# Kernel optimization log

Hardware: AMD Instinct MI355X
Metric: run time of the kernel (lower is better)

Reference implementation:

```python
import jax, jax.numpy as jnp
import numpy as np

N = 100000      # nodes
E = 1600000     # edges (avg degree 16)
F_IN = 64       # graph_input_dim
HID = 64        # gcn_out_dims (constant)
NG = 128        # number of graphs in batch
GF = 32         # global_input_dim
L1, L2, OUT = 256, 128, 1


def _glorot(k, fan_in, fan_out):
    s = 1.0 / np.sqrt(fan_in)
    return jax.random.uniform(k, (fan_in, fan_out), jnp.float32, -s, s)


def setup_inputs() -> dict:
    key = jax.random.key(0)
    ks = jax.random.split(key, 20)
    x = jax.random.normal(ks[0], (N, F_IN), jnp.float32)
    edge_index = jax.random.randint(ks[1], (2, E), 0, N, jnp.int64)
    # every graph gets a contiguous, non-empty slice of nodes (sorted batch ids)
    batch = (jnp.arange(N, dtype=jnp.int64) * NG) // N
    global_features = jax.random.normal(ks[2], (NG, GF), jnp.float32)
    dims = [F_IN, HID, HID, HID]
    inp = {"x": x, "global_features": global_features}
    for i in range(3):
        inp[f"conv_w{i+1}"] = _glorot(ks[3 + i], dims[i], dims[i + 1])
        inp[f"conv_b{i+1}"] = jnp.zeros((dims[i + 1],), jnp.float32)
    inp["fc_w1"] = _glorot(ks[8], HID * 2 + GF, L1)
    inp["fc_b1"] = jnp.zeros((L1,), jnp.float32)
    inp["fc_w2"] = _glorot(ks[9], L1, L2)
    inp["fc_b2"] = jnp.zeros((L2,), jnp.float32)
    inp["out_w"] = _glorot(ks[10], L2, OUT)
    inp["out_b"] = jnp.zeros((OUT,), jnp.float32)
    inp["edge_index"] = edge_index
    inp["batch"] = batch
    return inp


def _gcn_conv(x, src, dst, w, b, n):
    """PyG GCNConv: x' = D^-1/2 (A + I) D^-1/2 (x W) + b."""
    h = x @ w  # [n, out]
    loop = jnp.arange(n, dtype=src.dtype)
    s = jnp.concatenate([src, loop])
    d = jnp.concatenate([dst, loop])
    deg = jax.ops.segment_sum(jnp.ones(s.shape, h.dtype), d, num_segments=n)
    dinv = jnp.where(deg > 0, jax.lax.rsqrt(deg), 0.0)
    norm = dinv[s] * dinv[d]  # [E+n]
    out = jax.ops.segment_sum(h[s] * norm[:, None], d, num_segments=n)
    return out + b


def _forward(x, global_features, conv_w1, conv_b1, conv_w2, conv_b2,
             conv_w3, conv_b3, fc_w1, fc_b1, fc_w2, fc_b2, out_w, out_b,
             edge_index, batch):
    src, dst = edge_index[0], edge_index[1]
    n = x.shape[0]
    ng = global_features.shape[0]
    for w, b in ((conv_w1, conv_b1), (conv_w2, conv_b2), (conv_w3, conv_b3)):
        x = jax.nn.leaky_relu(_gcn_conv(x, src, dst, w, b, n))
    counts = jax.ops.segment_sum(jnp.ones((n,), x.dtype), batch, num_segments=ng)
    mean_pool = jax.ops.segment_sum(x, batch, num_segments=ng) / counts[:, None]
    max_pool = jax.ops.segment_max(x, batch, num_segments=ng)
    h = jnp.concatenate([mean_pool, max_pool, global_features], axis=1)
    h = jax.nn.leaky_relu(h @ fc_w1 + fc_b1)
    h = jax.nn.leaky_relu(h @ fc_w2 + fc_b2)
    return h @ out_w + out_b


def reference(x, global_features, conv_w1, conv_b1, conv_w2, conv_b2,
              conv_w3, conv_b3, fc_w1, fc_b1, fc_w2, fc_b2, out_w, out_b,
              edge_index, batch):
    return _forward(x, global_features, conv_w1, conv_b1, conv_w2, conv_b2,
                    conv_w3, conv_b3, fc_w1, fc_b1, fc_w2, fc_b2, out_w, out_b,
                    edge_index, batch)
```

## Files before the change

### kernel.cpp

```cpp
#include <hip/hip_runtime.h>
#include <hip/hip_fp16.h>
#include <stdint.h>

#define LRELU(x) ((x) > 0.0f ? (x) : 0.01f * (x))

struct h4 { __half2 a, b; };
struct h8 { __half2 a, b, c, d; };

typedef _Float16 f16x8 __attribute__((ext_vector_type(8)));
typedef float    f32x4 __attribute__((ext_vector_type(4)));

#define EPB 8192
#define PARTS 16


__global__ __launch_bounds__(256) void hist1_kernel(const int* __restrict__ dst,
                                                    int* __restrict__ bhist,
                                                    int nblk, int E, int nbk) {
    __shared__ int h[512];
    int blk = blockIdx.x, t = threadIdx.x;
    for (int i = t; i < nbk; i += 256) h[i] = 0;
    __syncthreads();
    #pragma unroll
    for (int k = 0; k < EPB / 1024; ++k) {
        int i4 = blk * (EPB / 4) + k * 256 + t;
        int e = i4 * 4;
        if (e + 3 < E) {
            int4 d = ((const int4*)dst)[i4];
            atomicAdd(&h[d.x >> 8], 1);
            atomicAdd(&h[d.y >> 8], 1);
            atomicAdd(&h[d.z >> 8], 1);
            atomicAdd(&h[d.w >> 8], 1);
        } else {
            for (int j = e; j < E; ++j) atomicAdd(&h[dst[j] >> 8], 1);
        }
    }
    __syncthreads();
    for (int i = t; i < nbk; i += 256) bhist[i * nblk + blk] = h[i];
}

__global__ __launch_bounds__(256) void scanb_kernel(int* __restrict__ bhist,
                                                    int* __restrict__ btot, int nblk) {
    __shared__ int s[256];
    __shared__ int carry;
    int b = blockIdx.x, t = threadIdx.x;
    if (t == 0) carry = 0;
    __syncthreads();
    for (int c0 = 0; c0 < nblk; c0 += 256) {
        int idx = c0 + t;
        int v = (idx < nblk) ? bhist[b * nblk + idx] : 0;
        s[t] = v;
        __syncthreads();
        for (int off = 1; off < 256; off <<= 1) {
            int a = (t >= off) ? s[t - off] : 0;
            __syncthreads();
            s[t] += a;
            __syncthreads();
        }
        if (idx < nblk) bhist[b * nblk + idx] = s[t] - v + carry;
        __syncthreads();
        if (t == 255) carry += s[255];
        __syncthreads();
    }
    if (t == 0) btot[b] = carry;
}

__global__ __launch_bounds__(512) void bbase_wprep_kernel(const int* __restrict__ btot,
                                                          int* __restrict__ bbase,
                                                          int nbk, int E,
                                                          const float* __restrict__ w1,
                                                          const float* __restrict__ w2,
                                                          const float* __restrict__ w3,
                                                          _Float16* __restrict__ Bf) {
    if (blockIdx.x == 0) {
        __shared__ int s[512];
        int t = threadIdx.x;
        int v = (t < nbk) ? btot[t] : 0;
        s[t] = v;
        __syncthreads();
        for (int off = 1; off < 512; off <<= 1) {
            int a = (t >= off) ? s[t - off] : 0;
            __syncthreads();
            s[t] += a;
            __syncthreads();
        }
        if (t < nbk) bbase[t] = s[t] - v;
        if (t == 0) bbase[nbk] = E;
    } else {
        int bc = blockIdx.x - 1;
        int tid = threadIdx.x;
        if (tid < 256) {
            int layer = bc >> 1, c = bc & 1;
            const float* W = (layer == 0) ? w1 : ((layer == 1) ? w2 : w3);
            int t = tid >> 6, l = tid & 63;
            _Float16* dstp = Bf + ((size_t)(layer * 8 + c * 4 + t) * 64 + l) * 8;
            int n  = t * 16 + (l & 15);
            int kb = c * 32 + (l >> 4) * 8;
            #pragma unroll
            for (int i = 0; i < 8; ++i) dstp[i] = (_Float16)W[(kb + i) * 64 + n];
        }
    }
}

__global__ __launch_bounds__(256) void place_kernel(const int* __restrict__ src,
                                                    const int* __restrict__ dst,
                                                    const int* __restrict__ bbase,
                                                    const int* __restrict__ bhist,
                                                    unsigned* __restrict__ bedge,
                                                    int nblk, int E, int nbk) {
    __shared__ int cur[512];
    int blk = blockIdx.x, t = threadIdx.x;
    for (int i = t; i < nbk; i += 256) cur[i] = bbase[i] + bhist[i * nblk + blk];
    __syncthreads();
    #pragma unroll
    for (int k = 0; k < EPB / 1024; ++k) {
        int i4 = blk * (EPB / 4) + k * 256 + t;
        int e = i4 * 4;
        if (e + 3 < E) {
            int4 s4 = ((const int4*)src)[i4];
            int4 d4 = ((const int4*)dst)[i4];
            int p0 = atomicAdd(&cur[d4.x >> 8], 1);
            int p1 = atomicAdd(&cur[d4.y >> 8], 1);
            int p2 = atomicAdd(&cur[d4.z >> 8], 1);
            int p3 = atomicAdd(&cur[d4.w >> 8], 1);
            bedge[p0] = ((unsigned)s4.x << 8) | (unsigned)(d4.x & 255);
            bedge[p1] = ((unsigned)s4.y << 8) | (unsigned)(d4.y & 255);
            bedge[p2] = ((unsigned)s4.z << 8) | (unsigned)(d4.z & 255);
            bedge[p3] = ((unsigned)s4.w << 8) | (unsigned)(d4.w & 255);
        } else {
            for (int j = e; j < E; ++j) {
                int d = dst[j];
                int pos = atomicAdd(&cur[d >> 8], 1);
                bedge[pos] = ((unsigned)src[j] << 8) | (unsigned)(d & 255);
            }
        }
    }
}

__global__ __launch_bounds__(256) void csr_kernel(const unsigned* __restrict__ bedge,
                                                  const int* __restrict__ bbase,
                                                  int* __restrict__ row_ptr,
                                                  float* __restrict__ dinv,
                                                  int* __restrict__ csr_src,
                                                  const int* __restrict__ batch,
                                                  int* __restrict__ gstart,
                                                  int N, int E, int nbk, int NG) {
    __shared__ int cnt[256];
    __shared__ int s[256];
    __shared__ int cur[256];
    int b = blockIdx.x, t = threadIdx.x;
    int node0 = b << 8;
    int beg = bbase[b], end = bbase[b + 1];
    cnt[t] = 0;
    __syncthreads();
    for (int i = beg + t; i < end; i += 256) atomicAdd(&cnt[bedge[i] & 255u], 1);
    __syncthreads();
    int c = cnt[t];
    s[t] = c;
    __syncthreads();
    for (int off = 1; off < 256; off <<= 1) {
        int a = (t >= off) ? s[t - off] : 0;
        __syncthreads();
        s[t] += a;
        __syncthreads();
    }
    int rp = beg + s[t] - c;
    int node = node0 + t;
    if (node < N) {
        row_ptr[node] = rp;
        dinv[node] = rsqrtf((float)c + 1.0f);
        int bb = batch[node];
        if (node == 0) {
            gstart[bb] = 0;
            gstart[NG] = N;
        } else if (batch[node - 1] != bb) {
            gstart[bb] = node;
        }
    }
    cur[t] = rp;
    if (b == nbk - 1 && t == 0) row_ptr[N] = E;
    __syncthreads();
    for (int i = beg + t; i < end; i += 256) {
        unsigned u = bedge[i];
        int pos = atomicAdd(&cur[u & 255u], 1);
        csr_src[pos] = (int)(u >> 8);
    }
}


template <bool XF32>
__global__ __launch_bounds__(256) void gemm_mfma_kernel(const void* __restrict__ Xv,
                                                        const _Float16* __restrict__ Bf,
                                                        const float* __restrict__ dinv,
                                                        __half* __restrict__ H, int N) {
    int w = threadIdx.x >> 6;
    int l = threadIdx.x & 63;
    int col = l & 15;
    int kg  = l >> 4;
    int base = blockIdx.x * 64 + w * 16;
    int nodeA = base + col;
    bool okA = nodeA < N;

    f32x4 acc[4] = {};
    #pragma unroll
    for (int c = 0; c < 2; ++c) {
        int k0 = c * 32 + kg * 8;
        f16x8 a = {};
        if (okA) {
            if constexpr (XF32) {
                const float* xp = (const float*)Xv + (size_t)nodeA * 64 + k0;
                float4 u = *(const float4*)xp;
                float4 v = *(const float4*)(xp + 4);
                a[0] = (_Float16)u.x; a[1] = (_Float16)u.y;
                a[2] = (_Float16)u.z; a[3] = (_Float16)u.w;
                a[4] = (_Float16)v.x; a[5] = (_Float16)v.y;
                a[6] = (_Float16)v.z; a[7] = (_Float16)v.w;
            } else {
                a = *(const f16x8*)((const __half*)Xv + (size_t)nodeA * 64 + k0);
            }
        }
        #pragma unroll
        for (int t = 0; t < 4; ++t) {
            f16x8 b = *(const f16x8*)(Bf + ((size_t)(c * 4 + t) * 64 + l) * 8);
            acc[t] = __builtin_amdgcn_mfma_f32_16x16x32_f16(a, b, acc[t], 0, 0, 0);
        }
    }
    float dvr[4];
    int rowN[4];
    #pragma unroll
    for (int r = 0; r < 4; ++r) {
        rowN[r] = base + kg * 4 + r;
        dvr[r] = (rowN[r] < N) ? dinv[rowN[r]] : 0.0f;
    }
    #pragma unroll
    for (int t = 0; t < 4; ++t) {
        #pragma unroll
        for (int r = 0; r < 4; ++r) {
            if (rowN[r] < N)
                H[(size_t)rowN[r] * 64 + t * 16 + col] = __float2half(acc[t][r] * dvr[r]);
        }
    }
}

#define ACC8(vv, c0, c1, c2, c3, c4, c5, c6, c7)                                \
    { float2 p;                                                                 \
      p = __half22float2((vv).a); c0 += p.x; c1 += p.y;                         \
      p = __half22float2((vv).b); c2 += p.x; c3 += p.y;                         \
      p = __half22float2((vv).c); c4 += p.x; c5 += p.y;                         \
      p = __half22float2((vv).d); c6 += p.x; c7 += p.y; }

__global__ __launch_bounds__(256) void agg_kernel(const __half* __restrict__ H,
                                                  const int* __restrict__ rp,
                                                  const int* __restrict__ csrc,
                                                  const float* __restrict__ dinv,
                                                  const float* __restrict__ bias,
                                                  __half* __restrict__ Y, int N) {
    int w = (blockIdx.x * blockDim.x + threadIdx.x) >> 6;
    int nA = w << 1;
    if (nA >= N) return;
    int nB = nA + 1;
    bool hasB = nB < N;
    int l = threadIdx.x & 63;
    int slot = l >> 3;
    int fo = (l & 7) << 3;
    int endA = rp[nA + 1];
    int eA = rp[nA] + slot;
    int endB = hasB ? rp[nB + 1] : 0;
    int eB = hasB ? (rp[nB] + slot) : 0;
    float a0=0,a1=0,a2=0,a3=0,a4=0,a5=0,a6=0,a7=0;
    float b0=0,b1=0,b2=0,b3=0,b4=0,b5=0,b6=0,b7=0;
    while (eA + 8 < endA && eB + 8 < endB) {
        int sA0 = csrc[eA], sA1 = csrc[eA + 8];
        int sB0 = csrc[eB], sB1 = csrc[eB + 8];
        h8 vA0 = *(const h8*)&H[(size_t)sA0 * 64 + fo];
        h8 vA1 = *(const h8*)&H[(size_t)sA1 * 64 + fo];
        h8 vB0 = *(const h8*)&H[(size_t)sB0 * 64 + fo];
        h8 vB1 = *(const h8*)&H[(size_t)sB1 * 64 + fo];
        ACC8(vA0, a0,a1,a2,a3,a4,a5,a6,a7);
        ACC8(vA1, a0,a1,a2,a3,a4,a5,a6,a7);
        ACC8(vB0, b0,b1,b2,b3,b4,b5,b6,b7);
        ACC8(vB1, b0,b1,b2,b3,b4,b5,b6,b7);
        eA += 16; eB += 16;
    }
    while (eA + 8 < endA) {
        int s0 = csrc[eA], s1 = csrc[eA + 8];
        h8 v0 = *(const h8*)&H[(size_t)s0 * 64 + fo];
        h8 v1 = *(const h8*)&H[(size_t)s1 * 64 + fo];
        ACC8(v0, a0,a1,a2,a3,a4,a5,a6,a7);
        ACC8(v1, a0,a1,a2,a3,a4,a5,a6,a7);
        eA += 16;
    }
    while (eB + 8 < endB) {
        int s0 = csrc[eB], s1 = csrc[eB + 8];
        h8 v0 = *(const h8*)&H[(size_t)s0 * 64 + fo];
        h8 v1 = *(const h8*)&H[(size_t)s1 * 64 + fo];
        ACC8(v0, b0,b1,b2,b3,b4,b5,b6,b7);
        ACC8(v1, b0,b1,b2,b3,b4,b5,b6,b7);
        eB += 16;
    }
    if (eA < endA) {
        h8 v0 = *(const h8*)&H[(size_t)csrc[eA] * 64 + fo];
        ACC8(v0, a0,a1,a2,a3,a4,a5,a6,a7);
    }
    if (eB < endB) {
        h8 v0 = *(const h8*)&H[(size_t)csrc[eB] * 64 + fo];
        ACC8(v0, b0,b1,b2,b3,b4,b5,b6,b7);
    }
    #pragma unroll
    for (int m = 8; m <= 32; m <<= 1) {
        a0 += __shfl_xor(a0, m); a1 += __shfl_xor(a1, m);
        a2 += __shfl_xor(a2, m); a3 += __shfl_xor(a3, m);
        a4 += __shfl_xor(a4, m); a5 += __shfl_xor(a5, m);
        a6 += __shfl_xor(a6, m); a7 += __shfl_xor(a7, m);
        b0 += __shfl_xor(b0, m); b1 += __shfl_xor(b1, m);
        b2 += __shfl_xor(b2, m); b3 += __shfl_xor(b3, m);
        b4 += __shfl_xor(b4, m); b5 += __shfl_xor(b5, m);
        b6 += __shfl_xor(b6, m); b7 += __shfl_xor(b7, m);
    }
    if (l < 8) {
        float4 bv0 = *(const float4*)&bias[fo];
        float4 bv1 = *(const float4*)&bias[fo + 4];
        {
            h8 hs = *(const h8*)&H[(size_t)nA * 64 + fo];
            float2 s0 = __half22float2(hs.a), s1 = __half22float2(hs.b);
            float2 s2 = __half22float2(hs.c), s3 = __half22float2(hs.d);
            float dv = dinv[nA];
            float o0 = LRELU(dv * (a0 + s0.x) + bv0.x);
            float o1 = LRELU(dv * (a1 + s0.y) + bv0.y);
            float o2 = LRELU(dv * (a2 + s1.x) + bv0.z);
            float o3 = LRELU(dv * (a3 + s1.y) + bv0.w);
            float o4 = LRELU(dv * (a4 + s2.x) + bv1.x);
            float o5 = LRELU(dv * (a5 + s2.y) + bv1.y);
            float o6 = LRELU(dv * (a6 + s3.x) + bv1.z);
            float o7 = LRELU(dv * (a7 + s3.y) + bv1.w);
            h8 o;
            o.a = __floats2half2_rn(o0, o1);
            o.b = __floats2half2_rn(o2, o3);
            o.c = __floats2half2_rn(o4, o5);
            o.d = __floats2half2_rn(o6, o7);
            *(h8*)&Y[(size_t)nA * 64 + fo] = o;
        }
        if (hasB) {
            h8 hs = *(const h8*)&H[(size_t)nB * 64 + fo];
            float2 s0 = __half22float2(hs.a), s1 = __half22float2(hs.b);
            float2 s2 = __half22float2(hs.c), s3 = __half22float2(hs.d);
            float dv = dinv[nB];
            float o0 = LRELU(dv * (b0 + s0.x) + bv0.x);
            float o1 = LRELU(dv * (b1 + s0.y) + bv0.y);
            float o2 = LRELU(dv * (b2 + s1.x) + bv0.z);
            float o3 = LRELU(dv * (b3 + s1.y) + bv0.w);
            float o4 = LRELU(dv * (b4 + s2.x) + bv1.x);
            float o5 = LRELU(dv * (b5 + s2.y) + bv1.y);
            float o6 = LRELU(dv * (b6 + s3.x) + bv1.z);
            float o7 = LRELU(dv * (b7 + s3.y) + bv1.w);
            h8 o;
            o.a = __floats2half2_rn(o0, o1);
            o.b = __floats2half2_rn(o2, o3);
            o.c = __floats2half2_rn(o4, o5);
            o.d = __floats2half2_rn(o6, o7);
            *(h8*)&Y[(size_t)nB * 64 + fo] = o;
        }
    }
}


__global__ __launch_bounds__(256) void pool1_kernel(const __half* __restrict__ Y,
                                                    const int* __restrict__ gstart,
                                                    float* __restrict__ pbuf) {
    __shared__ float ssum[8][64];
    __shared__ float smax[8][64];
    int g = blockIdx.x / PARTS;
    int p = blockIdx.x % PARTS;
    int t = threadIdx.x;
    int f2 = (t & 31) * 2;
    int rg = t >> 5;
    int s = gstart[g], epos = gstart[g + 1];
    int len = epos - s;
    int lo = s + (int)((long long)len * p / PARTS);
    int hi = s + (int)((long long)len * (p + 1) / PARTS);
    float sx = 0.f, sy = 0.f, mx = -3.0e38f, my = -3.0e38f;
    for (int r = lo + rg; r < hi; r += 8) {
        __half2 v = *(const __half2*)&Y[(size_t)r * 64 + f2];
        float2 f = __half22float2(v);
        sx += f.x; sy += f.y;
        mx = fmaxf(mx, f.x); my = fmaxf(my, f.y);
    }
    ssum[rg][f2] = sx; ssum[rg][f2 + 1] = sy;
    smax[rg][f2] = mx; smax[rg][f2 + 1] = my;
    __syncthreads();
    if (t < 64) {
        float ts = 0.f, tm = -3.0e38f;
        #pragma unroll
        for (int r = 0; r < 8; ++r) {
            ts += ssum[r][t];
            tm = fmaxf(tm, smax[r][t]);
        }
        float* row = &pbuf[(size_t)(g * PARTS + p) * 128];
        row[t] = ts;
        row[64 + t] = tm;
    }
}

__global__ __launch_bounds__(256) void mlp_kernel(const float* __restrict__ pbuf,
                                                  const int* __restrict__ gstart,
                                                  const float* __restrict__ gfeat,
                                                  const float* __restrict__ w1,
                                                  const float* __restrict__ b1,
                                                  const float* __restrict__ w2,
                                                  const float* __restrict__ b2,
                                                  const float* __restrict__ w3,
                                                  const float* __restrict__ b3,
                                                  float* __restrict__ out, int NG) {
    __shared__ float hl[160];
    __shared__ float h1[256];
    __shared__ float red[128];
    int g = blockIdx.x, t = threadIdx.x;
    if (t < 64) {
        const float* base = &pbuf[(size_t)g * PARTS * 128];
        float ts = 0.f, tm = -3.0e38f;
        #pragma unroll
        for (int p = 0; p < PARTS; ++p) {
            ts += base[p * 128 + t];
            tm = fmaxf(tm, base[p * 128 + 64 + t]);
        }
        float cnt = (float)(gstart[g + 1] - gstart[g]);
        hl[t] = ts / cnt;
        hl[64 + t] = tm;
    } else if (t >= 128 && t < 160) {
        hl[t] = gfeat[g * 32 + (t - 128)];
    }
    __syncthreads();
    float a1 = b1[t];
    for (int k = 0; k < 160; ++k) a1 += hl[k] * w1[k * 256 + t];
    h1[t] = LRELU(a1);
    __syncthreads();
    if (t < 128) {
        float a2 = b2[t];
        for (int k = 0; k < 256; ++k) a2 += h1[k] * w2[k * 128 + t];
        red[t] = LRELU(a2) * w3[t];
    }
    __syncthreads();
    if (t == 0) {
        float a3 = b3[0];
        for (int k = 0; k < 128; ++k) a3 += red[k];
        out[g] = a3;
    }
}


extern "C" void kernel_launch(void* const* d_in, const int* in_sizes, int n_in,
                              void* d_out, int out_size, void* d_ws, size_t ws_size,
                              hipStream_t stream) {
    const float* x      = (const float*)d_in[0];
    const float* gfeat  = (const float*)d_in[1];
    const float* cw1    = (const float*)d_in[2];
    const float* cb1    = (const float*)d_in[3];
    const float* cw2    = (const float*)d_in[4];
    const float* cb2    = (const float*)d_in[5];
    const float* cw3    = (const float*)d_in[6];
    const float* cb3    = (const float*)d_in[7];
    const float* fw1    = (const float*)d_in[8];
    const float* fb1    = (const float*)d_in[9];
    const float* fw2    = (const float*)d_in[10];
    const float* fb2    = (const float*)d_in[11];
    const float* ow     = (const float*)d_in[12];
    const float* ob     = (const float*)d_in[13];
    const int*   eidx   = (const int*)d_in[14];
    const int*   batch  = (const int*)d_in[15];

    const int N    = in_sizes[0] / 64;
    const int E    = in_sizes[14] / 2;
    const int NG   = in_sizes[1] / 32;
    const int NBUK = (N + 255) >> 8;
    const int NBLK = (E + EPB - 1) / EPB;
    const int* src = eidx;
    const int* dst = eidx + E;

    char* wp = (char*)d_ws;
    auto carve = [&](size_t bytes) {
        void* p = (void*)wp;
        wp += (bytes + 255) & ~(size_t)255;
        return p;
    };
    float*     dinv    = (float*)    carve((size_t)N * 4);
    int*       row_ptr = (int*)      carve((size_t)(N + 1) * 4);
    int*       bhist   = (int*)      carve((size_t)NBUK * NBLK * 4);
    int*       btot    = (int*)      carve((size_t)NBUK * 4);
    int*       bbase   = (int*)      carve((size_t)(NBUK + 1) * 4);
    unsigned*  bedge   = (unsigned*) carve((size_t)E * 4);
    int*       csr_src = (int*)      carve((size_t)E * 4);
    __half*    hbuf    = (__half*)   carve((size_t)N * 64 * 2);
    __half*    ybuf    = (__half*)   carve((size_t)N * 64 * 2);
    int*       gstart  = (int*)      carve((size_t)(NG + 1) * 4);
    float*     pbuf    = (float*)    carve((size_t)NG * PARTS * 128 * 4);
    _Float16*  Bf      = (_Float16*) carve((size_t)3 * 4096 * 2);
    float*     outf    = (float*)d_out;

    hist1_kernel<<<NBLK, 256, 0, stream>>>(dst, bhist, NBLK, E, NBUK);
    scanb_kernel<<<NBUK, 256, 0, stream>>>(bhist, btot, NBLK);
    bbase_wprep_kernel<<<7, 512, 0, stream>>>(btot, bbase, NBUK, E, cw1, cw2, cw3, Bf);
    place_kernel<<<NBLK, 256, 0, stream>>>(src, dst, bbase, bhist, bedge, NBLK, E, NBUK);
    csr_kernel<<<NBUK, 256, 0, stream>>>(bedge, bbase, row_ptr, dinv, csr_src,
                                         batch, gstart, N, E, NBUK, NG);

    const int gemmB = (N + 63) / 64;
    const int aggB  = ((N + 1) / 2 + 3) / 4;

    gemm_mfma_kernel<true ><<<gemmB, 256, 0, stream>>>(x,    Bf,        dinv, hbuf, N);
    agg_kernel<<<aggB, 256, 0, stream>>>(hbuf, row_ptr, csr_src, dinv, cb1, ybuf, N);
    gemm_mfma_kernel<false><<<gemmB, 256, 0, stream>>>(ybuf, Bf + 4096, dinv, hbuf, N);
    agg_kernel<<<aggB, 256, 0, stream>>>(hbuf, row_ptr, csr_src, dinv, cb2, ybuf, N);
    gemm_mfma_kernel<false><<<gemmB, 256, 0, stream>>>(ybuf, Bf + 8192, dinv, hbuf, N);
    agg_kernel<<<aggB, 256, 0, stream>>>(hbuf, row_ptr, csr_src, dinv, cb3, ybuf, N);

    pool1_kernel<<<NG * PARTS, 256, 0, stream>>>(ybuf, gstart, pbuf);
    mlp_kernel<<<NG, 256, 0, stream>>>(pbuf, gstart, gfeat, fw1, fb1, fw2, fb2, ow, ob, outf, NG);
}
```

Measured before the change: 219.8 us.

## Fuse GCN aggregation with next layer's MFMA GEMM via LDS tile

Adds agg_gemm_kernel, which aggregates neighbor features for 16 nodes per block, applies bias and leaky ReLU, stores the result in LDS, then runs the next layer's 64x64 MFMA GEMM on that tile and writes the dinv-scaled output. Layers 1 and 2 now use this kernel with ping-pong H buffers, which removes two GEMM launches and the round trip of the intermediate Y through global memory. In exchange, each block holds only 16 nodes, half its waves sit idle during the GEMM phase, and a block-wide barrier separates the gather from the GEMM. This could lower latency hiding in the gather-bound aggregation.

```diff
diff --git a/kernel.cpp b/kernel.cpp
--- a/kernel.cpp
+++ b/kernel.cpp
@@ -188,8 +188,7 @@
 }
 
 
-template <bool XF32>
-__global__ __launch_bounds__(256) void gemm_mfma_kernel(const void* __restrict__ Xv,
+__global__ __launch_bounds__(256) void gemm_mfma_kernel(const float* __restrict__ X,
                                                         const _Float16* __restrict__ Bf,
                                                         const float* __restrict__ dinv,
                                                         __half* __restrict__ H, int N) {
@@ -207,17 +206,13 @@
         int k0 = c * 32 + kg * 8;
         f16x8 a = {};
         if (okA) {
-            if constexpr (XF32) {
-                const float* xp = (const float*)Xv + (size_t)nodeA * 64 + k0;
-                float4 u = *(const float4*)xp;
-                float4 v = *(const float4*)(xp + 4);
-                a[0] = (_Float16)u.x; a[1] = (_Float16)u.y;
-                a[2] = (_Float16)u.z; a[3] = (_Float16)u.w;
-                a[4] = (_Float16)v.x; a[5] = (_Float16)v.y;
-                a[6] = (_Float16)v.z; a[7] = (_Float16)v.w;
-            } else {
-                a = *(const f16x8*)((const __half*)Xv + (size_t)nodeA * 64 + k0);
-            }
+            const float* xp = X + (size_t)nodeA * 64 + k0;
+            float4 u = *(const float4*)xp;
+            float4 v = *(const float4*)(xp + 4);
+            a[0] = (_Float16)u.x; a[1] = (_Float16)u.y;
+            a[2] = (_Float16)u.z; a[3] = (_Float16)u.w;
+            a[4] = (_Float16)v.x; a[5] = (_Float16)v.y;
+            a[6] = (_Float16)v.z; a[7] = (_Float16)v.w;
         }
         #pragma unroll
         for (int t = 0; t < 4; ++t) {
@@ -248,6 +243,133 @@
       p = __half22float2((vv).b); c2 += p.x; c3 += p.y;                         \
       p = __half22float2((vv).c); c4 += p.x; c5 += p.y;                         \
       p = __half22float2((vv).d); c6 += p.x; c7 += p.y; }
+
+__global__ __launch_bounds__(512) void agg_gemm_kernel(const __half* __restrict__ H,
+                                                       const int* __restrict__ rp,
+                                                       const int* __restrict__ csrc,
+                                                       const float* __restrict__ dinv,
+                                                       const float* __restrict__ bias,
+                                                       const _Float16* __restrict__ Bf,
+                                                       __half* __restrict__ Hout, int N) {
+    __shared__ _Float16 ylds[16][72];
+    int wv = threadIdx.x >> 6;
+    int l  = threadIdx.x & 63;
+    int base = blockIdx.x * 16;
+    int nA = base + wv * 2;
+    int nB = nA + 1;
+    bool hasA = nA < N;
+    bool hasB = nB < N;
+    int slot = l >> 3;
+    int fo = (l & 7) << 3;
+    float a0=0,a1=0,a2=0,a3=0,a4=0,a5=0,a6=0,a7=0;
+    float b0=0,b1=0,b2=0,b3=0,b4=0,b5=0,b6=0,b7=0;
+    if (hasA) {
+        int endA = rp[nA + 1];
+        int eA = rp[nA] + slot;
+        int endB = hasB ? rp[nB + 1] : 0;
+        int eB = hasB ? (rp[nB] + slot) : 0;
+        while (eA + 8 < endA && eB + 8 < endB) {
+            int sA0 = csrc[eA], sA1 = csrc[eA + 8];
+            int sB0 = csrc[eB], sB1 = csrc[eB + 8];
+            h8 vA0 = *(const h8*)&H[(size_t)sA0 * 64 + fo];
+            h8 vA1 = *(const h8*)&H[(size_t)sA1 * 64 + fo];
+            h8 vB0 = *(const h8*)&H[(size_t)sB0 * 64 + fo];
+            h8 vB1 = *(const h8*)&H[(size_t)sB1 * 64 + fo];
+            ACC8(vA0, a0,a1,a2,a3,a4,a5,a6,a7);
+            ACC8(vA1, a0,a1,a2,a3,a4,a5,a6,a7);
+            ACC8(vB0, b0,b1,b2,b3,b4,b5,b6,b7);
+            ACC8(vB1, b0,b1,b2,b3,b4,b5,b6,b7);
+            eA += 16; eB += 16;
+        }
+        while (eA + 8 < endA) {
+            int s0 = csrc[eA], s1 = csrc[eA + 8];
+            h8 v0 = *(const h8*)&H[(size_t)s0 * 64 + fo];
+            h8 v1 = *(const h8*)&H[(size_t)s1 * 64 + fo];
+            ACC8(v0, a0,a1,a2,a3,a4,a5,a6,a7);
+            ACC8(v1, a0,a1,a2,a3,a4,a5,a6,a7);
+            eA += 16;
+        }
+        while (eB + 8 < endB) {
+            int s0 = csrc[eB], s1 = csrc[eB + 8];
+            h8 v0 = *(const h8*)&H[(size_t)s0 * 64 + fo];
+            h8 v1 = *(const h8*)&H[(size_t)s1 * 64 + fo];
+            ACC8(v0, b0,b1,b2,b3,b4,b5,b6,b7);
+            ACC8(v1, b0,b1,b2,b3,b4,b5,b6,b7);
+            eB += 16;
+        }
+        if (eA < endA) {
+            h8 v0 = *(const h8*)&H[(size_t)csrc[eA] * 64 + fo];
+            ACC8(v0, a0,a1,a2,a3,a4,a5,a6,a7);
+        }
+        if (eB < endB) {
+            h8 v0 = *(const h8*)&H[(size_t)csrc[eB] * 64 + fo];
+            ACC8(v0, b0,b1,b2,b3,b4,b5,b6,b7);
+        }
+        #pragma unroll
+        for (int m = 8; m <= 32; m <<= 1) {
+            a0 += __shfl_xor(a0, m); a1 += __shfl_xor(a1, m);
+            a2 += __shfl_xor(a2, m); a3 += __shfl_xor(a3, m);
+            a4 += __shfl_xor(a4, m); a5 += __shfl_xor(a5, m);
+            a6 += __shfl_xor(a6, m); a7 += __shfl_xor(a7, m);
+            b0 += __shfl_xor(b0, m); b1 += __shfl_xor(b1, m);
+            b2 += __shfl_xor(b2, m); b3 += __shfl_xor(b3, m);
+            b4 += __shfl_xor(b4, m); b5 += __shfl_xor(b5, m);
+            b6 += __shfl_xor(b6, m); b7 += __shfl_xor(b7, m);
+        }
+        if (l < 8) {
+            float4 bv0 = *(const float4*)&bias[fo];
+            float4 bv1 = *(const float4*)&bias[fo + 4];
+            {
+                h8 hs = *(const h8*)&H[(size_t)nA * 64 + fo];
+                float2 s0 = __half22float2(hs.a), s1 = __half22float2(hs.b);
+                float2 s2 = __half22float2(hs.c), s3 = __half22float2(hs.d);
+                float dv = dinv[nA];
+                _Float16* yp = &ylds[wv * 2][fo];
+                yp[0] = (_Float16)(LRELU(dv * (a0 + s0.x) + bv0.x));
+                yp[1] = (_Float16)(LRELU(dv * (a1 + s0.y) + bv0.y));
+                yp[2] = (_Float16)(LRELU(dv * (a2 + s1.x) + bv0.z));
+                yp[3] = (_Float16)(LRELU(dv * (a3 + s1.y) + bv0.w));
+                yp[4] = (_Float16)(LRELU(dv * (a4 + s2.x) + bv1.x));
+                yp[5] = (_Float16)(LRELU(dv * (a5 + s2.y) + bv1.y));
+                yp[6] = (_Float16)(LRELU(dv * (a6 + s3.x) + bv1.z));
+                yp[7] = (_Float16)(LRELU(dv * (a7 + s3.y) + bv1.w));
+            }
+            if (hasB) {
+                h8 hs = *(const h8*)&H[(size_t)nB * 64 + fo];
+                float2 s0 = __half22float2(hs.a), s1 = __half22float2(hs.b);
+                float2 s2 = __half22float2(hs.c), s3 = __half22float2(hs.d);
+                float dv = dinv[nB];
+                _Float16* yp = &ylds[wv * 2 + 1][fo];
+                yp[0] = (_Float16)(LRELU(dv * (b0 + s0.x) + bv0.x));
+                yp[1] = (_Float16)(LRELU(dv * (b1 + s0.y) + bv0.y));
+                yp[2] = (_Float16)(LRELU(dv * (b2 + s1.x) + bv0.z));
+                yp[3] = (_Float16)(LRELU(dv * (b3 + s1.y) + bv0.w));
+                yp[4] = (_Float16)(LRELU(dv * (b4 + s2.x) + bv1.x));
+                yp[5] = (_Float16)(LRELU(dv * (b5 + s2.y) + bv1.y));
+                yp[6] = (_Float16)(LRELU(dv * (b6 + s3.x) + bv1.z));
+                yp[7] = (_Float16)(LRELU(dv * (b7 + s3.y) + bv1.w));
+            }
+        }
+    }
+    __syncthreads();
+    if (wv < 4) {
+        int col = l & 15;
+        int kg  = l >> 4;
+        f32x4 acc = {};
+        #pragma unroll
+        for (int c = 0; c < 2; ++c) {
+            f16x8 a = *(const f16x8*)&ylds[col][c * 32 + kg * 8];
+            f16x8 b = *(const f16x8*)(Bf + ((size_t)(c * 4 + wv) * 64 + l) * 8);
+            acc = __builtin_amdgcn_mfma_f32_16x16x32_f16(a, b, acc, 0, 0, 0);
+        }
+        #pragma unroll
+        for (int r = 0; r < 4; ++r) {
+            int row = base + kg * 4 + r;
+            if (row < N)
+                Hout[(size_t)row * 64 + wv * 16 + col] = __float2half(acc[r] * dinv[row]);
+        }
+    }
+}
 
 __global__ __launch_bounds__(256) void agg_kernel(const __half* __restrict__ H,
                                                   const int* __restrict__ rp,
@@ -489,7 +611,8 @@
     int*       bbase   = (int*)      carve((size_t)(NBUK + 1) * 4);
     unsigned*  bedge   = (unsigned*) carve((size_t)E * 4);
     int*       csr_src = (int*)      carve((size_t)E * 4);
-    __half*    hbuf    = (__half*)   carve((size_t)N * 64 * 2);
+    __half*    hA      = (__half*)   carve((size_t)N * 64 * 2);
+    __half*    hB      = (__half*)   carve((size_t)N * 64 * 2);
     __half*    ybuf    = (__half*)   carve((size_t)N * 64 * 2);
     int*       gstart  = (int*)      carve((size_t)(NG + 1) * 4);
     float*     pbuf    = (float*)    carve((size_t)NG * PARTS * 128 * 4);
@@ -503,15 +626,16 @@
     csr_kernel<<<NBUK, 256, 0, stream>>>(bedge, bbase, row_ptr, dinv, csr_src,
                                          batch, gstart, N, E, NBUK, NG);
 
-    const int gemmB = (N + 63) / 64;
-    const int aggB  = ((N + 1) / 2 + 3) / 4;
-
-    gemm_mfma_kernel<true ><<<gemmB, 256, 0, stream>>>(x,    Bf,        dinv, hbuf, N);
-    agg_kernel<<<aggB, 256, 0, stream>>>(hbuf, row_ptr, csr_src, dinv, cb1, ybuf, N);
-    gemm_mfma_kernel<false><<<gemmB, 256, 0, stream>>>(ybuf, Bf + 4096, dinv, hbuf, N);
-    agg_kernel<<<aggB, 256, 0, stream>>>(hbuf, row_ptr, csr_src, dinv, cb2, ybuf, N);
-    gemm_mfma_kernel<false><<<gemmB, 256, 0, stream>>>(ybuf, Bf + 8192, dinv, hbuf, N);
-    agg_kernel<<<aggB, 256, 0, stream>>>(hbuf, row_ptr, csr_src, dinv, cb3, ybuf, N);
+    const int gemmB  = (N + 63) / 64;
+    const int fuseB  = (N + 15) / 16;
+    const int aggB   = ((N + 1) / 2 + 3) / 4;
+
+    gemm_mfma_kernel<<<gemmB, 256, 0, stream>>>(x, Bf, dinv, hA, N);
+    agg_gemm_kernel<<<fuseB, 512, 0, stream>>>(hA, row_ptr, csr_src, dinv, cb1,
+                                               Bf + 4096, hB, N);
+    agg_gemm_kernel<<<fuseB, 512, 0, stream>>>(hB, row_ptr, csr_src, dinv, cb2,
+                                               Bf + 8192, hA, N);
+    agg_kernel<<<aggB, 256, 0, stream>>>(hA, row_ptr, csr_src, dinv, cb3, ybuf, N);
 
     pool1_kernel<<<NG * PARTS, 256, 0, stream>>>(ybuf, gstart, pbuf);
     mlp_kernel<<<NG, 256, 0, stream>>>(pbuf, gstart, gfeat, fw1, fb1, fw2, fb2, ow, ob, outf, NG);
```

Measured after the change: 211.8 us. 1.04x faster.
